# Performance work log

Measured on AMD Instinct MI355X. Metric: run time of the kernel, lower is better.

Reference implementation:

```python
import jax, jax.numpy as jnp
import numpy as np

D_MODEL = 32; D_STATE = 16; D_CONV = 4; D_INNER = 64; DT_RANK = 2
BATCH = 64; C_IN = 64; PATCH = 32; FEATURE_DIM = 128


def setup_inputs() -> dict:
    key = jax.random.key(0)
    ks = jax.random.split(key, 14)
    def w(k, shape, fan_in):
        return jax.random.normal(k, shape, jnp.float32) * np.float32(1.0 / np.sqrt(fan_in))
    dt_init = jnp.exp(jax.random.uniform(ks[12], (D_INNER,), jnp.float32,
                                         np.float32(np.log(1e-3)), np.float32(np.log(1e-1))))
    return {
        "x": jax.random.normal(ks[0], (BATCH, C_IN, PATCH, PATCH), jnp.float32),
        "conv_w": w(ks[1], (D_MODEL, C_IN), C_IN),
        "conv_b": jnp.zeros((D_MODEL,), jnp.float32),
        "bn_gamma": jnp.ones((D_MODEL,), jnp.float32),
        "bn_beta": jnp.zeros((D_MODEL,), jnp.float32),
        "bn_mean": jnp.zeros((D_MODEL,), jnp.float32),
        "bn_var": jnp.ones((D_MODEL,), jnp.float32),
        "in_proj_w": w(ks[2], (2 * D_INNER, D_MODEL), D_MODEL),
        "conv1d_w": w(ks[3], (D_INNER, D_CONV), D_CONV),
        "conv1d_b": jnp.zeros((D_INNER,), jnp.float32),
        "x_proj_w": w(ks[4], (DT_RANK + 2 * D_STATE, D_INNER), D_INNER),
        "dt_proj_w": w(ks[5], (D_INNER, DT_RANK), DT_RANK),
        "dt_proj_b": jnp.log(jnp.expm1(dt_init)),
        "A_log": jnp.log(jnp.tile(jnp.arange(1, D_STATE + 1, dtype=jnp.float32), (D_INNER, 1))),
        "D_param": jnp.ones((D_INNER,), jnp.float32),
        "out_proj_w": w(ks[6], (D_MODEL, D_INNER), D_INNER),
        "fc_w": w(ks[7], (FEATURE_DIM, D_MODEL), D_MODEL),
        "fc_b": jnp.zeros((FEATURE_DIM,), jnp.float32),
    }


def reference(x, conv_w, conv_b, bn_gamma, bn_beta, bn_mean, bn_var, in_proj_w,
              conv1d_w, conv1d_b, x_proj_w, dt_proj_w, dt_proj_b, A_log, D_param,
              out_proj_w, fc_w, fc_b):
    Bsz = x.shape[0]
    # --- stem: 1x1 conv + BatchNorm (eval stats) + exact GELU ---
    h = jnp.einsum('bchw,dc->bdhw', x, conv_w) + conv_b[:, None, None]
    scale = bn_gamma / jnp.sqrt(bn_var + 1e-5)
    h = (h - bn_mean[:, None, None]) * scale[:, None, None] + bn_beta[:, None, None]
    h = jax.nn.gelu(h, approximate=False)
    u = h.reshape(Bsz, D_MODEL, -1).transpose(0, 2, 1)   # [B, L, d_model], L = H*W
    # --- Mamba block ---
    xz = u @ in_proj_w.T                                  # [B, L, 2*d_inner]
    xm, z = xz[..., :D_INNER], xz[..., D_INNER:]
    # depthwise causal conv1d over the sequence
    xt = jnp.pad(xm.transpose(0, 2, 1), ((0, 0), (0, 0), (D_CONV - 1, 0)))
    xt = jax.lax.conv_general_dilated(xt, conv1d_w[:, None, :], (1,), 'VALID',
                                      feature_group_count=D_INNER,
                                      dimension_numbers=('NCH', 'OIH', 'NCH'))
    xm = jax.nn.silu(xt + conv1d_b[None, :, None]).transpose(0, 2, 1)  # [B, L, d_inner]
    x_dbl = xm @ x_proj_w.T                               # [B, L, dt_rank + 2*d_state]
    dt = jax.nn.softplus(x_dbl[..., :DT_RANK] @ dt_proj_w.T + dt_proj_b)  # [B, L, d_inner]
    Bt = x_dbl[..., DT_RANK:DT_RANK + D_STATE]            # [B, L, d_state]
    Ct = x_dbl[..., DT_RANK + D_STATE:]                   # [B, L, d_state]
    A = -jnp.exp(A_log)                                   # [d_inner, d_state]

    def step(hst, inp):
        u_t, dt_t, B_t, C_t = inp                         # [B,d],[B,d],[B,n],[B,n]
        hst = jnp.exp(dt_t[:, :, None] * A) * hst + (dt_t * u_t)[:, :, None] * B_t[:, None, :]
        return hst, jnp.einsum('bdn,bn->bd', hst, C_t)

    h0 = jnp.zeros((Bsz, D_INNER, D_STATE), xm.dtype)
    _, ys = jax.lax.scan(step, h0, (xm.transpose(1, 0, 2), dt.transpose(1, 0, 2),
                                    Bt.transpose(1, 0, 2), Ct.transpose(1, 0, 2)))
    y = ys.transpose(1, 0, 2) + xm * D_param
    y = y * jax.nn.silu(z)
    out = y @ out_proj_w.T                                # [B, L, d_model]
    pooled = out.mean(axis=1)                             # [B, d_model]
    return pooled @ fc_w.T + fc_b                         # [B, FEATURE_DIM]
```

## Files before the change

kernel.cpp:

```cpp
#include <hip/hip_runtime.h>
#include <hip/hip_bf16.h>
#include <math.h>

#define L 1024
typedef __hip_bfloat16 bf;
typedef __attribute__((ext_vector_type(8))) short short8v;
typedef __attribute__((ext_vector_type(4))) short short4v;

__device__ __forceinline__ float b2f(bf v) { return __bfloat162float(v); }
__device__ __forceinline__ bf f2b(float v) { return __float2bfloat16(v); }
__device__ __forceinline__ float bits2f(short s) {
  union { unsigned u; float f; } cv; cv.u = ((unsigned)(unsigned short)s) << 16; return cv.f;
}
union Pack4 { short4v v; unsigned short e[4]; };
union Pack8 { short8v v; unsigned short e[8]; };
__device__ __forceinline__ unsigned short f2bits(float v) {
  union { bf b; unsigned short u; } cv; cv.b = __float2bfloat16(v); return cv.u;
}

__global__ __launch_bounds__(256, 2) void k_front(
    const float* __restrict__ x, const float* __restrict__ conv_w,
    const float* __restrict__ conv_b, const float* __restrict__ gamma,
    const float* __restrict__ beta, const float* __restrict__ mean,
    const float* __restrict__ var, const float* __restrict__ ipw,
    bf* __restrict__ xm, bf* __restrict__ z) {
  __shared__ float xs[64 * 65];
  __shared__ float hsh[64][34];
  int t = threadIdx.x;
  int b = blockIdx.x >> 4;
  int l0 = (blockIdx.x & 15) << 6;
  const float* xg = x + (size_t)b * 65536 + l0;
#pragma unroll
  for (int k = 0; k < 16; ++k) {
    int i = t + k * 256;
    int c = i >> 6, ll = i & 63;
    xs[c * 65 + ll] = xg[(size_t)c * L + ll];
  }
  __syncthreads();
  int lq = t & 63;
  int q = __builtin_amdgcn_readfirstlane(t >> 6);
  int l = l0 | lq;
  float hacc[8];
#pragma unroll
  for (int dd = 0; dd < 8; ++dd) hacc[dd] = conv_b[q * 8 + dd];
#pragma unroll
  for (int c4 = 0; c4 < 16; ++c4) {
    float x0 = xs[(c4 * 4 + 0) * 65 + lq];
    float x1 = xs[(c4 * 4 + 1) * 65 + lq];
    float x2 = xs[(c4 * 4 + 2) * 65 + lq];
    float x3 = xs[(c4 * 4 + 3) * 65 + lq];
#pragma unroll
    for (int dd = 0; dd < 8; ++dd) {
      const float* w = conv_w + (q * 8 + dd) * 64 + c4 * 4;
      hacc[dd] = fmaf(x0, w[0], fmaf(x1, w[1],
                 fmaf(x2, w[2], fmaf(x3, w[3], hacc[dd]))));
    }
  }
#pragma unroll
  for (int dd = 0; dd < 8; ++dd) {
    int d = q * 8 + dd;
    float sc = gamma[d] * rsqrtf(var[d] + 1e-5f);
    float acc = (hacc[dd] - mean[d]) * sc + beta[d];
    hsh[lq][d] = 0.5f * acc * (1.0f + erff(acc * 0.70710678118654752f));
  }
  __syncthreads();
  float h[32];
#pragma unroll
  for (int d = 0; d < 32; ++d) h[d] = hsh[lq][d];
  if (q < 2) {
    short8v* xr8 = (short8v*)(xm + ((size_t)b * 1024 + l) * 64) + q * 4;
#pragma unroll
    for (int j8 = 0; j8 < 4; ++j8) {
      Pack8 p;
#pragma unroll
      for (int e = 0; e < 8; ++e) {
        int j = q * 32 + j8 * 8 + e;
        float acc = 0.f;
#pragma unroll
        for (int d = 0; d < 32; ++d) acc = fmaf(h[d], ipw[j * 32 + d], acc);
        p.e[e] = f2bits(acc);
      }
      xr8[j8] = p.v;
    }
  } else {
    bf* zp = z + (size_t)b * 65536 + l;
#pragma unroll
    for (int jj = 0; jj < 32; ++jj) {
      int j = (q - 2) * 32 + jj;
      float acc = 0.f;
#pragma unroll
      for (int d = 0; d < 32; ++d) acc = fmaf(h[d], ipw[(j + 64) * 32 + d], acc);
      zp[(size_t)j * L] = f2b(acc);
    }
  }
}

__global__ __launch_bounds__(256, 2) void k_mid(
    const bf* __restrict__ xm, const float* __restrict__ c1w,
    const float* __restrict__ c1b, const float* __restrict__ xpw,
    const float* __restrict__ dtw, const float* __restrict__ dtbp,
    bf* __restrict__ u, bf* __restrict__ dt_o,
    bf* __restrict__ Bt, bf* __restrict__ Ct) {
  __shared__ float ush[64][65];
  int t = threadIdx.x;
  int lq = t & 63;
  int q = __builtin_amdgcn_readfirstlane(t >> 6);
  int b = blockIdx.x >> 4;
  int l = ((blockIdx.x & 15) << 6) | lq;
  float um[16];
#pragma unroll
  for (int dd = 0; dd < 16; ++dd) um[dd] = c1b[q * 16 + dd];
#pragma unroll
  for (int k = 0; k < 4; ++k) {
    int lr = l - 3 + k;
    if (lr >= 0) {
      const short8v* row = (const short8v*)(xm + ((size_t)b * 1024 + lr) * 64 + q * 16);
      short8v v0 = row[0], v1 = row[1];
#pragma unroll
      for (int e = 0; e < 8; ++e) {
        um[e]     = fmaf(c1w[(q * 16 + e) * 4 + k],     bits2f(v0[e]), um[e]);
        um[8 + e] = fmaf(c1w[(q * 16 + 8 + e) * 4 + k], bits2f(v1[e]), um[8 + e]);
      }
    }
  }
  {
    bf* up = u + (size_t)b * 65536 + l;
#pragma unroll
    for (int dd = 0; dd < 16; ++dd) {
      float s = um[dd];
      s = s / (1.f + __expf(-s));
      ush[lq][q * 16 + dd] = s;
      up[(size_t)(q * 16 + dd) * L] = f2b(s);
    }
  }
  __syncthreads();
  float um64[64];
#pragma unroll
  for (int d = 0; d < 64; ++d) um64[d] = ush[lq][d];
  int i = l & 31, c = l >> 5;
  size_t basei = ((size_t)b * 16384 + (size_t)i * 128 + c * 4) >> 2;
  if (q == 0) {
    float xd0 = 0.f, xd1 = 0.f;
#pragma unroll
    for (int d = 0; d < 64; ++d) {
      xd0 = fmaf(um64[d], xpw[d], xd0);
      xd1 = fmaf(um64[d], xpw[64 + d], xd1);
    }
    bf* dp = dt_o + (size_t)b * 65536 + l;
#pragma unroll
    for (int d = 0; d < 64; ++d) {
      float raw = fmaf(xd0, dtw[d * 2], fmaf(xd1, dtw[d * 2 + 1], dtbp[d]));
      float sp = fmaxf(raw, 0.f) + log1pf(__expf(-fabsf(raw)));
      dp[(size_t)d * L] = f2b(sp);
    }
  } else {
    short4v* B4 = (short4v*)Bt;
    short4v* C4 = (short4v*)Ct;
#pragma unroll
    for (int job = 0; job < 3; ++job) {
      int kb, n4; short4v* dst;
      if (q == 1)      { if (job == 0) { dst = B4; kb = 2;  n4 = 0; }
                         else if (job == 1) { dst = B4; kb = 6;  n4 = 1; }
                         else { dst = C4; kb = 18; n4 = 0; } }
      else if (q == 2) { if (job == 0) { dst = B4; kb = 10; n4 = 2; }
                         else if (job == 1) { dst = B4; kb = 14; n4 = 3; }
                         else { dst = C4; kb = 22; n4 = 1; } }
      else             { if (job == 0) { dst = C4; kb = 26; n4 = 2; }
                         else if (job == 1) { dst = C4; kb = 30; n4 = 3; }
                         else break; }
      Pack4 p;
#pragma unroll
      for (int nn = 0; nn < 4; ++nn) {
        float acc = 0.f;
#pragma unroll
        for (int d = 0; d < 64; ++d) acc = fmaf(um64[d], xpw[(kb + nn) * 64 + d], acc);
        p.e[nn] = f2bits(acc);
      }
      dst[basei + (size_t)n4 * 1024] = p.v;
    }
  }
}

__global__ __launch_bounds__(256, 2) void k_scan(
    const bf* __restrict__ u, const bf* __restrict__ dt,
    const bf* __restrict__ z, const bf* __restrict__ Bt,
    const bf* __restrict__ Ct, const float* __restrict__ A_log,
    const float* __restrict__ Dp, float* __restrict__ pooled64) {
  __shared__ bf Bsh[16384];
  __shared__ bf Csh[16384];
  int phys = blockIdx.x;
  int b = phys & 63;
  int dgrp = phys >> 6;
  int t = threadIdx.x;
  int d_local = t >> 5, c = t & 31;
  int d = dgrp * 8 + d_local;
  int g = b * 64 + d;

  {
    const short8v* Bg8 = (const short8v*)(Bt + (size_t)b * 16384);
    const short8v* Cg8 = (const short8v*)(Ct + (size_t)b * 16384);
    short8v* Bs8 = (short8v*)Bsh;
    short8v* Cs8 = (short8v*)Csh;
#pragma unroll
    for (int q = 0; q < 8; ++q) {
      Bs8[t + q * 256] = Bg8[t + q * 256];
      Cs8[t + q * 256] = Cg8[t + q * 256];
    }
  }
  __syncthreads();

  float An[16];
#pragma unroll
  for (int n = 0; n < 16; ++n) An[n] = -__expf(A_log[d * 16 + n]);
  const short4v* dps = (const short4v*)(dt + (size_t)g * L + c * 32);
  const short4v* ups = (const short4v*)(u  + (size_t)g * L + c * 32);
  const short4v* zps = (const short4v*)(z  + (size_t)g * L + c * 32);
  const short4v* Bs4 = (const short4v*)Bsh;
  const short4v* Cs4 = (const short4v*)Csh;
  float Dd = Dp[d];

  float h[16], pi[16], q[16];
#pragma unroll
  for (int n = 0; n < 16; ++n) { h[n] = 0.f; pi[n] = 1.f; q[n] = 0.f; }
  float base = 0.f;

#pragma unroll 1
  for (int t4 = 0; t4 < 8; ++t4) {
    short4v d4 = dps[t4], u4 = ups[t4], z4 = zps[t4];
#pragma unroll
    for (int i = 0; i < 4; ++i) {
      int step = t4 * 4 + i;
      float dtv = bits2f(d4[i]);
      float uv  = bits2f(u4[i]);
      float zv  = bits2f(z4[i]);
      float sv  = zv / (1.f + __expf(-zv));
      float du  = dtv * uv;
      int slot = step * 32 + c;
      float y0 = 0.f, y1 = 0.f;
#pragma unroll
      for (int n4 = 0; n4 < 4; ++n4) {
        short4v bq = Bs4[n4 * 1024 + slot];
        short4v cq = Cs4[n4 * 1024 + slot];
#pragma unroll
        for (int nn = 0; nn < 4; ++nn) {
          int n = n4 * 4 + nn;
          float a = __expf(dtv * An[n]);
          float Bv = bits2f(bq[nn]);
          float Cv = bits2f(cq[nn]);
          h[n] = fmaf(a, h[n], du * Bv);
          pi[n] *= a;
          if (nn & 1) y1 = fmaf(h[n], Cv, y1); else y0 = fmaf(h[n], Cv, y0);
          q[n] = fmaf(sv * pi[n], Cv, q[n]);
        }
      }
      base = fmaf(sv, (y0 + y1) + uv * Dd, base);
    }
  }

#pragma unroll
  for (int s = 1; s < 32; s <<= 1) {
    bool act = (c >= s);
#pragma unroll
    for (int n = 0; n < 16; ++n) {
      float Po = __shfl_up(pi[n], (unsigned)s, 32);
      float Oo = __shfl_up(h[n], (unsigned)s, 32);
      if (act) { h[n] = fmaf(pi[n], Oo, h[n]); pi[n] *= Po; }
    }
  }
  float pooled = base;
#pragma unroll
  for (int n = 0; n < 16; ++n) {
    float v = __shfl_up(h[n], 1u, 32);
    float hin = (c == 0) ? 0.f : v;
    pooled = fmaf(q[n], hin, pooled);
  }
#pragma unroll
  for (int s = 1; s < 32; s <<= 1) pooled += __shfl_xor(pooled, s, 32);
  if (c == 0) pooled64[g] = pooled;
}

__global__ __launch_bounds__(128) void k_fc(
    const float* __restrict__ pooled64, const float* __restrict__ opw,
    const float* __restrict__ fcw, const float* __restrict__ fcb,
    float* __restrict__ out) {
  __shared__ float p64[64];
  __shared__ float o32[32];
  int b = blockIdx.x, t = threadIdx.x;
  if (t < 64) p64[t] = pooled64[b * 64 + t];
  __syncthreads();
  if (t < 32) {
    float s = 0.f;
#pragma unroll
    for (int d0 = 0; d0 < 64; ++d0) s = fmaf(p64[d0], opw[t * 64 + d0], s);
    o32[t] = s * (1.f / 1024.f);
  }
  __syncthreads();
  float acc = fcb[t];
#pragma unroll
  for (int j = 0; j < 32; ++j) acc = fmaf(o32[j], fcw[t * 32 + j], acc);
  out[b * 128 + t] = acc;
}

extern "C" void kernel_launch(void* const* d_in, const int* in_sizes, int n_in,
                              void* d_out, int out_size, void* d_ws, size_t ws_size,
                              hipStream_t stream) {
  const float* x      = (const float*)d_in[0];
  const float* conv_w = (const float*)d_in[1];
  const float* conv_b = (const float*)d_in[2];
  const float* bn_g   = (const float*)d_in[3];
  const float* bn_b   = (const float*)d_in[4];
  const float* bn_m   = (const float*)d_in[5];
  const float* bn_v   = (const float*)d_in[6];
  const float* ipw    = (const float*)d_in[7];
  const float* c1w    = (const float*)d_in[8];
  const float* c1b    = (const float*)d_in[9];
  const float* xpw    = (const float*)d_in[10];
  const float* dtw    = (const float*)d_in[11];
  const float* dtbp   = (const float*)d_in[12];
  const float* A_log  = (const float*)d_in[13];
  const float* Dp     = (const float*)d_in[14];
  const float* opw    = (const float*)d_in[15];
  const float* fcw    = (const float*)d_in[16];
  const float* fcb    = (const float*)d_in[17];

  char* ws = (char*)d_ws;
  bf* xmb = (bf*)(ws + 0);
  bf* zb  = (bf*)(ws + 8388608);
  bf* ub  = (bf*)(ws + 16777216);
  bf* dtb = (bf*)(ws + 25165824);
  bf* Btb = (bf*)(ws + 33554432);
  bf* Ctb = (bf*)(ws + 35651584);
  float* pooled = (float*)(ws + 37748736);

  hipLaunchKernelGGL(k_front, dim3(1024), dim3(256), 0, stream,
                     x, conv_w, conv_b, bn_g, bn_b, bn_m, bn_v, ipw, xmb, zb);
  hipLaunchKernelGGL(k_mid, dim3(1024), dim3(256), 0, stream,
                     xmb, c1w, c1b, xpw, dtw, dtbp, ub, dtb, Btb, Ctb);
  hipLaunchKernelGGL(k_scan, dim3(512), dim3(256), 0, stream,
                     ub, dtb, zb, Btb, Ctb, A_log, Dp, pooled);
  hipLaunchKernelGGL(k_fc, dim3(64), dim3(128), 0, stream,
                     pooled, opw, fcw, fcb, (float*)d_out);
}
```

Measured before the change: 130.3 us.

## Balance k_mid work across waves and stage inputs and x_proj weights in LDS

Rewrites k_mid so the four waves split the 34 x_proj outputs evenly (9/9/8/8) and the 64-channel softplus dt computation (16 each), instead of wave 0 doing all the dt work. Each wave writes its partial results to a shared xdh buffer and then packs B/C from it. The conv1d input rows with halo, and the x_proj weights, are staged cooperatively into LDS so the convolution and projection no longer re-read global memory per thread. This costs more shared memory, which may lower occupancy, plus an extra barrier.

```diff
diff --git a/kernel.cpp b/kernel.cpp
--- a/kernel.cpp
+++ b/kernel.cpp
@@ -101,26 +101,43 @@
     const float* __restrict__ dtw, const float* __restrict__ dtbp,
     bf* __restrict__ u, bf* __restrict__ dt_o,
     bf* __restrict__ Bt, bf* __restrict__ Ct) {
-  __shared__ float ush[64][65];
+  __shared__ bf    xsh[67 * 68];
+  __shared__ float wsh[34 * 64];
+  __shared__ float ush[64 * 65];
+  __shared__ float xdh[64 * 35];
   int t = threadIdx.x;
   int lq = t & 63;
   int q = __builtin_amdgcn_readfirstlane(t >> 6);
   int b = blockIdx.x >> 4;
-  int l = ((blockIdx.x & 15) << 6) | lq;
+  int l0 = (blockIdx.x & 15) << 6;
+  int l = l0 | lq;
+  {
+    const short4v* xg4 = (const short4v*)(xm + ((size_t)b * 1024 + l0 - 3) * 64);
+    for (int i = t; i < 1072; i += 256) {
+      int r = i >> 4, c4 = i & 15;
+      short4v v;
+      if (l0 == 0 && r < 3) { v[0] = v[1] = v[2] = v[3] = 0; }
+      else v = xg4[i];
+      *(short4v*)(&xsh[r * 68 + c4 * 4]) = v;
+    }
+    const float4* wg = (const float4*)xpw;
+    float4* ws4 = (float4*)wsh;
+    for (int i = t; i < 544; i += 256) ws4[i] = wg[i];
+  }
+  __syncthreads();
   float um[16];
 #pragma unroll
   for (int dd = 0; dd < 16; ++dd) um[dd] = c1b[q * 16 + dd];
 #pragma unroll
   for (int k = 0; k < 4; ++k) {
-    int lr = l - 3 + k;
-    if (lr >= 0) {
-      const short8v* row = (const short8v*)(xm + ((size_t)b * 1024 + lr) * 64 + q * 16);
-      short8v v0 = row[0], v1 = row[1];
-#pragma unroll
-      for (int e = 0; e < 8; ++e) {
-        um[e]     = fmaf(c1w[(q * 16 + e) * 4 + k],     bits2f(v0[e]), um[e]);
-        um[8 + e] = fmaf(c1w[(q * 16 + 8 + e) * 4 + k], bits2f(v1[e]), um[8 + e]);
-      }
+    const short4v* xr = (const short4v*)(&xsh[(lq + k) * 68 + q * 16]);
+#pragma unroll
+    for (int c4 = 0; c4 < 4; ++c4) {
+      short4v v = xr[c4];
+#pragma unroll
+      for (int e = 0; e < 4; ++e)
+        um[c4 * 4 + e] = fmaf(c1w[(q * 16 + c4 * 4 + e) * 4 + k],
+                              bits2f(v[e]), um[c4 * 4 + e]);
     }
   }
   {
@@ -129,55 +146,53 @@
     for (int dd = 0; dd < 16; ++dd) {
       float s = um[dd];
       s = s / (1.f + __expf(-s));
-      ush[lq][q * 16 + dd] = s;
+      ush[lq * 65 + q * 16 + dd] = s;
       up[(size_t)(q * 16 + dd) * L] = f2b(s);
     }
   }
   __syncthreads();
-  float um64[64];
-#pragma unroll
-  for (int d = 0; d < 64; ++d) um64[d] = ush[lq][d];
-  int i = l & 31, c = l >> 5;
-  size_t basei = ((size_t)b * 16384 + (size_t)i * 128 + c * 4) >> 2;
-  if (q == 0) {
-    float xd0 = 0.f, xd1 = 0.f;
-#pragma unroll
-    for (int d = 0; d < 64; ++d) {
-      xd0 = fmaf(um64[d], xpw[d], xd0);
-      xd1 = fmaf(um64[d], xpw[64 + d], xd1);
-    }
+  {
+    float um64[64];
+#pragma unroll
+    for (int d = 0; d < 64; ++d) um64[d] = ush[lq * 65 + d];
+    int k0 = (q < 2) ? q * 9 : 18 + (q - 2) * 8;
+    int nk = (q < 2) ? 9 : 8;
+    for (int kk = 0; kk < nk; ++kk) {
+      int k = k0 + kk;
+      const float4* wr = (const float4*)(&wsh[k * 64]);
+      float acc = 0.f;
+#pragma unroll
+      for (int d4 = 0; d4 < 16; ++d4) {
+        float4 w4 = wr[d4];
+        acc = fmaf(um64[d4 * 4 + 0], w4.x, fmaf(um64[d4 * 4 + 1], w4.y,
+              fmaf(um64[d4 * 4 + 2], w4.z, fmaf(um64[d4 * 4 + 3], w4.w, acc))));
+      }
+      xdh[lq * 35 + k] = acc;
+    }
+  }
+  __syncthreads();
+  {
+    float xd0 = xdh[lq * 35 + 0], xd1 = xdh[lq * 35 + 1];
     bf* dp = dt_o + (size_t)b * 65536 + l;
 #pragma unroll
-    for (int d = 0; d < 64; ++d) {
+    for (int dd = 0; dd < 16; ++dd) {
+      int d = q * 16 + dd;
       float raw = fmaf(xd0, dtw[d * 2], fmaf(xd1, dtw[d * 2 + 1], dtbp[d]));
       float sp = fmaxf(raw, 0.f) + log1pf(__expf(-fabsf(raw)));
       dp[(size_t)d * L] = f2b(sp);
     }
-  } else {
+    int i = l & 31, c = l >> 5;
+    size_t basei = ((size_t)b * 16384 + (size_t)i * 128 + c * 4) >> 2;
     short4v* B4 = (short4v*)Bt;
     short4v* C4 = (short4v*)Ct;
-#pragma unroll
-    for (int job = 0; job < 3; ++job) {
-      int kb, n4; short4v* dst;
-      if (q == 1)      { if (job == 0) { dst = B4; kb = 2;  n4 = 0; }
-                         else if (job == 1) { dst = B4; kb = 6;  n4 = 1; }
-                         else { dst = C4; kb = 18; n4 = 0; } }
-      else if (q == 2) { if (job == 0) { dst = B4; kb = 10; n4 = 2; }
-                         else if (job == 1) { dst = B4; kb = 14; n4 = 3; }
-                         else { dst = C4; kb = 22; n4 = 1; } }
-      else             { if (job == 0) { dst = C4; kb = 26; n4 = 2; }
-                         else if (job == 1) { dst = C4; kb = 30; n4 = 3; }
-                         else break; }
-      Pack4 p;
-#pragma unroll
-      for (int nn = 0; nn < 4; ++nn) {
-        float acc = 0.f;
-#pragma unroll
-        for (int d = 0; d < 64; ++d) acc = fmaf(um64[d], xpw[(kb + nn) * 64 + d], acc);
-        p.e[nn] = f2bits(acc);
-      }
-      dst[basei + (size_t)n4 * 1024] = p.v;
-    }
+    Pack4 pb, pc;
+#pragma unroll
+    for (int nn = 0; nn < 4; ++nn) {
+      pb.e[nn] = f2bits(xdh[lq * 35 + 2 + q * 4 + nn]);
+      pc.e[nn] = f2bits(xdh[lq * 35 + 18 + q * 4 + nn]);
+    }
+    B4[basei + (size_t)q * 1024] = pb.v;
+    C4[basei + (size_t)q * 1024] = pc.v;
   }
 }
 
```

Result: faster. 109.6 us (-15.9%).
